# Kernel tuning notes

Measured on AMD Instinct MI355X. Metric: run time of the kernel, lower is better.

## Reference

```python
import jax, jax.numpy as jnp
import numpy as np

NUM_ITERATIONS = 5
M_CHECKS, N_CODE, ROW_WEIGHT = 63, 127, 8
BATCH = 4096
BIG = 1e10  # sentinel used by optimized_topk for masked-out entries


def _make_H():
    # Deterministic sparse parity-check matrix with fixed row weight.
    rng = np.random.default_rng(0)
    H = np.zeros((M_CHECKS, N_CODE), dtype=np.int32)
    for i in range(M_CHECKS):
        H[i, rng.choice(N_CODE, ROW_WEIGHT, replace=False)] = 1
    return H


def setup_inputs() -> dict:
    key = jax.random.key(0)
    k1, k2 = jax.random.split(key)
    soft_input = jax.random.normal(k1, (BATCH, N_CODE), dtype=jnp.float32)
    labels = jax.random.randint(k2, (BATCH, N_CODE), 0, 2, dtype=jnp.int32)
    H = jnp.asarray(_make_H())
    normalizor = jnp.full((1,), -2.5, dtype=jnp.float32)  # decoder_check_normalizor
    return {"soft_input": soft_input, "labels": labels, "H": H,
            "normalizor": normalizor}


def _nms_iteration(cur, Hf, supp, norm):
    # variable -> check messages: (B, m, n)
    vc = cur[:, None, :] * Hf
    # sign part: product of signs over each check row, extrinsic per edge
    signs = jnp.sign(supp + vc)  # supplement makes masked entries sign +1
    total_sign = jnp.prod(signs, axis=2, keepdims=True) * Hf
    result_sign = total_sign * signs
    # magnitude part: extrinsic min via top-2 smallest magnitudes per row
    av = jnp.abs(vc)
    proc = jnp.where(av * Hf == 0.0, BIG, av * Hf)
    top2 = -jax.lax.top_k(-proc, 2)[0]           # (B, m, 2) two smallest
    smallest = top2[..., 0:1]
    second = top2[..., 1:2]
    updated = jnp.where(av == smallest, second, smallest) * Hf
    # normalized min-sum check -> variable messages
    cv = norm * updated * jax.lax.stop_gradient(result_sign)
    # marginalize: posterior = prior + sum of incoming check messages
    return cur + jnp.sum(cv, axis=1)


def reference(soft_input, labels, H, normalizor):
    Hf = H.astype(jnp.float32)                # (m, n)
    supp = (1.0 - Hf)[None]                   # supplement_matrix, (1, m, n)
    norm = jax.nn.softplus(normalizor)        # softplus(decoder_check_normalizor)
    outs = [soft_input]
    cur = soft_input
    for _ in range(NUM_ITERATIONS):
        cur = _nms_iteration(cur, Hf, supp, norm)
        outs.append(cur)
    return jnp.stack(outs, axis=0), labels    # (iters+1, B, n), (B, n)
```

## Files before the change

### kernel.cpp

```cpp
#include <hip/hip_runtime.h>
#include <math.h>

#define M_CHECKS 63
#define N_CODE   127
#define ROW_W    8
#define BATCH    4096
#define NITER    5
#define BIGF     1e10f
#define MAXD     16

__launch_bounds__(256, 4)
__global__ void nms_decode(const float* __restrict__ soft,
                           const int*   __restrict__ labels,
                           const int*   __restrict__ H,
                           const float* __restrict__ normalizor,
                           float*       __restrict__ out) {
    __shared__ float cur[4][128];
    __shared__ float cvals[4][MAXD / 2][128][2];
    __shared__ int   sidx[M_CHECKS * ROW_W];
    __shared__ int   sslot[M_CHECKS * ROW_W];
    __shared__ int   cnt[128];

    const int tid  = threadIdx.x;
    const int w    = tid >> 6;
    const int lane = tid & 63;
    const int row  = blockIdx.x * 4 + w;

    {
        float4* cv4 = (float4*)cvals;
        #pragma unroll
        for (int t = 0; t < (4 * MAXD * 128) / 4 / 256; ++t)
            cv4[tid + t * 256] = make_float4(0.f, 0.f, 0.f, 0.f);
        if (tid < 128) cnt[tid] = 0;
    }

    {
        const unsigned long long below =
            (lane == 0) ? 0ull : ((~0ull) >> (64 - lane));
        for (int i = w; i < M_CHECKS; i += 4) {
            const int c0 = lane;
            const int c1 = lane + 64;
            const int b0 = (H[i * N_CODE + c0] != 0) ? 1 : 0;
            const int b1 = (c1 < N_CODE) ? ((H[i * N_CODE + c1] != 0) ? 1 : 0) : 0;
            unsigned long long m0 = __ballot(b0);
            unsigned long long m1 = __ballot(b1);
            if (b0) {
                int pos = __popcll(m0 & below);
                if (pos < ROW_W) sidx[i * ROW_W + pos] = c0;
            }
            if (b1) {
                int pos = __popcll(m0) + __popcll(m1 & below);
                if (pos < ROW_W) sidx[i * ROW_W + pos] = c1;
            }
        }
    }
    __syncthreads();

    if (w == 0 && lane < M_CHECKS) {
        #pragma unroll
        for (int p = 0; p < ROW_W; ++p) {
            int c = sidx[lane * ROW_W + p];
            sslot[lane * ROW_W + p] = atomicAdd(&cnt[c], 1);
        }
    }
    __syncthreads();

    int dmax = max(cnt[lane], cnt[lane + 64]);
    #pragma unroll
    for (int off = 32; off; off >>= 1)
        dmax = max(dmax, __shfl_xor(dmax, off, 64));
    const int spairs = min((dmax + 1) >> 1, MAXD / 2);

    const float norm = log1pf(expf(normalizor[0]));
    float* outLabels = out + (size_t)(NITER + 1) * BATCH * N_CODE;
    float* const cvw = &cvals[w][0][0][0];

    int ec[ROW_W];
    int widx[ROW_W];
    if (lane < M_CHECKS) {
        #pragma unroll
        for (int p = 0; p < ROW_W; ++p) {
            int c   = sidx[lane * ROW_W + p];
            int s   = min(sslot[lane * ROW_W + p], MAXD - 1);
            ec[p]   = c;
            widx[p] = (s >> 1) * 256 + 2 * c + (s & 1);
        }
    }

    const int j0 = lane;
    const int j1 = lane + 64;
    float x0, x1 = 0.0f;
    {
        const size_t base = (size_t)row * N_CODE;
        x0 = soft[base + j0];
        cur[w][j0] = x0;
        out[base + j0] = x0;
        outLabels[base + j0] = (float)labels[base + j0];
        if (lane < 63) {
            x1 = soft[base + j1];
            cur[w][j1] = x1;
            out[base + j1] = x1;
            outLabels[base + j1] = (float)labels[base + j1];
        }
    }
    asm volatile("" ::: "memory");
    __builtin_amdgcn_sched_barrier(0);

    for (int it = 0; it < NITER; ++it) {
        if (lane < M_CHECKS) {
            float v[ROW_W];
            #pragma unroll
            for (int p = 0; p < ROW_W; ++p) v[p] = cur[w][ec[p]];

            float m1 = BIGF, m2 = BIGF, sprod = 1.0f;
            #pragma unroll
            for (int p = 0; p < ROW_W; ++p) {
                float x = v[p];
                float s = (x > 0.0f) ? 1.0f : ((x < 0.0f) ? -1.0f : 0.0f);
                sprod *= s;
                float av   = fabsf(x);
                float proc = (av == 0.0f) ? BIGF : av;
                if (proc < m1) { m2 = m1; m1 = proc; }
                else if (proc < m2) { m2 = proc; }
            }
            const float nsp = norm * sprod;
            #pragma unroll
            for (int p = 0; p < ROW_W; ++p) {
                float x   = v[p];
                float s   = (x > 0.0f) ? 1.0f : ((x < 0.0f) ? -1.0f : 0.0f);
                float av  = fabsf(x);
                float upd = (av == m1) ? m2 : m1;
                cvw[widx[p]] = nsp * upd * s;
            }
        }
        asm volatile("" ::: "memory");
        __builtin_amdgcn_sched_barrier(0);

        const float2* cv2 = (const float2*)cvw;
        float acc0 = 0.0f, acc1 = 0.0f;
        for (int e = 0; e < spairs; ++e) {
            float2 a = cv2[e * 128 + j0];
            float2 b = cv2[e * 128 + j1];
            acc0 += a.x + a.y;
            acc1 += b.x + b.y;
        }
        x0 += acc0;
        x1 += acc1;

        cur[w][j0] = x0;
        cur[w][j1] = x1;

        const size_t obase = (size_t)(it + 1) * BATCH * N_CODE + (size_t)row * N_CODE;
        out[obase + j0] = x0;
        if (lane < 63) out[obase + j1] = x1;

        asm volatile("" ::: "memory");
        __builtin_amdgcn_sched_barrier(0);
    }
}

extern "C" void kernel_launch(void* const* d_in, const int* in_sizes, int n_in,
                              void* d_out, int out_size, void* d_ws, size_t ws_size,
                              hipStream_t stream) {
    const float* soft       = (const float*)d_in[0];
    const int*   labels     = (const int*)d_in[1];
    const int*   H          = (const int*)d_in[2];
    const float* normalizor = (const float*)d_in[3];
    float*       out        = (float*)d_out;

    nms_decode<<<BATCH / 4, 256, 0, stream>>>(soft, labels, H, normalizor, out);
}
```

Baseline: 79.56 us.

## Precompute H edge tables in a separate kernel and use sign-bit arithmetic

Moves parsing of the parity-check matrix, the per-column slot assignment and the degree calculation out of every decode block into a one-block prepass kernel that writes a compact table to workspace. The decode kernel then loads its edge indices with vector loads and no longer needs block-wide barriers or shared-memory atomics; each wave zeroes only its own scratch. The check-node sign product is replaced with XOR of sign bits and a zero flag. In exchange it adds a second kernel launch with a serial dependency, and it relies on the workspace buffer being large enough.

Result: slower. 85.19 us (+7.1%).

```diff
diff --git a/kernel.cpp b/kernel.cpp
--- a/kernel.cpp
+++ b/kernel.cpp
@@ -9,17 +9,76 @@
 #define BIGF     1e10f
 #define MAXD     16
 
+__global__ void build_tables(const int* __restrict__ H, int* __restrict__ tbl) {
+    __shared__ int                sidx[M_CHECKS * ROW_W];
+    __shared__ unsigned long long cmask[128];
+
+    const int lane = threadIdx.x & 63;
+    const int c0 = lane;
+    const int c1 = lane + 64;
+    unsigned long long cm0 = 0ull, cm1 = 0ull;
+    const unsigned long long below =
+        (lane == 0) ? 0ull : ((~0ull) >> (64 - lane));
+
+    for (int k = 0; k < 4; ++k) {
+        int a[16], b[16];
+        #pragma unroll
+        for (int r = 0; r < 16; ++r) {
+            int i = k * 16 + r;
+            a[r] = (i < M_CHECKS) ? H[i * N_CODE + c0] : 0;
+            b[r] = (i < M_CHECKS && c1 < N_CODE) ? H[i * N_CODE + c1] : 0;
+        }
+        #pragma unroll
+        for (int r = 0; r < 16; ++r) {
+            int i = k * 16 + r;
+            if (i < M_CHECKS) {
+                unsigned long long m0 = __ballot(a[r] != 0);
+                unsigned long long m1 = __ballot(b[r] != 0);
+                if (a[r]) {
+                    int pos = __popcll(m0 & below);
+                    if (pos < ROW_W) sidx[i * ROW_W + pos] = c0;
+                }
+                if (b[r]) {
+                    int pos = __popcll(m0) + __popcll(m1 & below);
+                    if (pos < ROW_W) sidx[i * ROW_W + pos] = c1;
+                }
+                cm0 |= a[r] ? (1ull << i) : 0ull;
+                cm1 |= b[r] ? (1ull << i) : 0ull;
+            }
+        }
+    }
+    cmask[c0] = cm0;
+    cmask[c1 & 127] = cm1;
+
+    int deg = max(__popcll(cm0), __popcll(cm1));
+    #pragma unroll
+    for (int off = 32; off; off >>= 1)
+        deg = max(deg, __shfl_xor(deg, off, 64));
+
+    asm volatile("" ::: "memory");
+    __builtin_amdgcn_sched_barrier(0);
+
+    if (lane < M_CHECKS) {
+        const unsigned long long ibelow = (1ull << lane) - 1;
+        #pragma unroll
+        for (int p = 0; p < ROW_W; ++p) {
+            int c    = sidx[lane * ROW_W + p];
+            int slot = (int)__popcll(cmask[c] & ibelow);
+            tbl[lane * 16 + p]     = c;
+            tbl[lane * 16 + 8 + p] = (slot >> 1) * 256 + 2 * c + (slot & 1);
+        }
+    }
+    if (lane == 0) tbl[M_CHECKS * 16] = (deg + 1) >> 1;
+}
+
 __launch_bounds__(256, 4)
 __global__ void nms_decode(const float* __restrict__ soft,
                            const int*   __restrict__ labels,
-                           const int*   __restrict__ H,
                            const float* __restrict__ normalizor,
+                           const int*   __restrict__ tbl,
                            float*       __restrict__ out) {
     __shared__ float cur[4][128];
     __shared__ float cvals[4][MAXD / 2][128][2];
-    __shared__ int   sidx[M_CHECKS * ROW_W];
-    __shared__ int   sslot[M_CHECKS * ROW_W];
-    __shared__ int   cnt[128];
 
     const int tid  = threadIdx.x;
     const int w    = tid >> 6;
@@ -27,65 +86,26 @@
     const int row  = blockIdx.x * 4 + w;
 
     {
-        float4* cv4 = (float4*)cvals;
+        float4* z = (float4*)&cvals[w][0][0][0];
         #pragma unroll
-        for (int t = 0; t < (4 * MAXD * 128) / 4 / 256; ++t)
-            cv4[tid + t * 256] = make_float4(0.f, 0.f, 0.f, 0.f);
-        if (tid < 128) cnt[tid] = 0;
+        for (int t = 0; t < 8; ++t)
+            z[lane + t * 64] = make_float4(0.f, 0.f, 0.f, 0.f);
     }
 
+    int ec[ROW_W], widx[ROW_W];
     {
-        const unsigned long long below =
-            (lane == 0) ? 0ull : ((~0ull) >> (64 - lane));
-        for (int i = w; i < M_CHECKS; i += 4) {
-            const int c0 = lane;
-            const int c1 = lane + 64;
-            const int b0 = (H[i * N_CODE + c0] != 0) ? 1 : 0;
-            const int b1 = (c1 < N_CODE) ? ((H[i * N_CODE + c1] != 0) ? 1 : 0) : 0;
-            unsigned long long m0 = __ballot(b0);
-            unsigned long long m1 = __ballot(b1);
-            if (b0) {
-                int pos = __popcll(m0 & below);
-                if (pos < ROW_W) sidx[i * ROW_W + pos] = c0;
-            }
-            if (b1) {
-                int pos = __popcll(m0) + __popcll(m1 & below);
-                if (pos < ROW_W) sidx[i * ROW_W + pos] = c1;
-            }
-        }
+        const int4* t4 = (const int4*)(tbl + lane * 16);
+        int4 A = t4[0], B = t4[1], C = t4[2], D = t4[3];
+        ec[0] = A.x; ec[1] = A.y; ec[2] = A.z; ec[3] = A.w;
+        ec[4] = B.x; ec[5] = B.y; ec[6] = B.z; ec[7] = B.w;
+        widx[0] = C.x; widx[1] = C.y; widx[2] = C.z; widx[3] = C.w;
+        widx[4] = D.x; widx[5] = D.y; widx[6] = D.z; widx[7] = D.w;
     }
-    __syncthreads();
-
-    if (w == 0 && lane < M_CHECKS) {
-        #pragma unroll
-        for (int p = 0; p < ROW_W; ++p) {
-            int c = sidx[lane * ROW_W + p];
-            sslot[lane * ROW_W + p] = atomicAdd(&cnt[c], 1);
-        }
-    }
-    __syncthreads();
-
-    int dmax = max(cnt[lane], cnt[lane + 64]);
-    #pragma unroll
-    for (int off = 32; off; off >>= 1)
-        dmax = max(dmax, __shfl_xor(dmax, off, 64));
-    const int spairs = min((dmax + 1) >> 1, MAXD / 2);
+    const int spairs = __builtin_amdgcn_readfirstlane(tbl[M_CHECKS * 16]);
 
     const float norm = log1pf(expf(normalizor[0]));
     float* outLabels = out + (size_t)(NITER + 1) * BATCH * N_CODE;
     float* const cvw = &cvals[w][0][0][0];
-
-    int ec[ROW_W];
-    int widx[ROW_W];
-    if (lane < M_CHECKS) {
-        #pragma unroll
-        for (int p = 0; p < ROW_W; ++p) {
-            int c   = sidx[lane * ROW_W + p];
-            int s   = min(sslot[lane * ROW_W + p], MAXD - 1);
-            ec[p]   = c;
-            widx[p] = (s >> 1) * 256 + 2 * c + (s & 1);
-        }
-    }
 
     const int j0 = lane;
     const int j1 = lane + 64;
@@ -112,25 +132,26 @@
             #pragma unroll
             for (int p = 0; p < ROW_W; ++p) v[p] = cur[w][ec[p]];
 
-            float m1 = BIGF, m2 = BIGF, sprod = 1.0f;
+            float m1 = BIGF, m2 = BIGF;
+            unsigned xb = 0u;
+            bool anyz = false;
             #pragma unroll
             for (int p = 0; p < ROW_W; ++p) {
                 float x = v[p];
-                float s = (x > 0.0f) ? 1.0f : ((x < 0.0f) ? -1.0f : 0.0f);
-                sprod *= s;
-                float av   = fabsf(x);
-                float proc = (av == 0.0f) ? BIGF : av;
-                if (proc < m1) { m2 = m1; m1 = proc; }
-                else if (proc < m2) { m2 = proc; }
+                xb ^= __float_as_uint(x);
+                anyz |= (x == 0.0f);
+                float av = fabsf(x);
+                if (av < m1) { m2 = m1; m1 = av; }
+                else if (av < m2) { m2 = av; }
             }
-            const float nsp = norm * sprod;
+            const float    nsp = anyz ? 0.0f : norm;
+            const unsigned par = xb & 0x80000000u;
             #pragma unroll
             for (int p = 0; p < ROW_W; ++p) {
                 float x   = v[p];
-                float s   = (x > 0.0f) ? 1.0f : ((x < 0.0f) ? -1.0f : 0.0f);
-                float av  = fabsf(x);
-                float upd = (av == m1) ? m2 : m1;
-                cvw[widx[p]] = nsp * upd * s;
+                float upd = (fabsf(x) == m1) ? m2 : m1;
+                unsigned sb = (__float_as_uint(x) & 0x80000000u) ^ par;
+                cvw[widx[p]] = __uint_as_float(__float_as_uint(nsp * upd) ^ sb);
             }
         }
         asm volatile("" ::: "memory");
@@ -167,6 +188,8 @@
     const int*   H          = (const int*)d_in[2];
     const float* normalizor = (const float*)d_in[3];
     float*       out        = (float*)d_out;
+    int*         tbl        = (int*)d_ws;
 
-    nms_decode<<<BATCH / 4, 256, 0, stream>>>(soft, labels, H, normalizor, out);
+    build_tables<<<1, 64, 0, stream>>>(H, tbl);
+    nms_decode<<<BATCH / 4, 256, 0, stream>>>(soft, labels, normalizor, tbl, out);
 }
```

## Replace shared-memory state with wave shuffles and drop atomic slot assignment

Applied to the files above, without the earlier changes.

Removes the per-wave shared `cur` array and gathers variable values with cross-lane shuffles. It also replaces the atomic per-column slot counting, and the extra block barrier it needed, with per-column check bitmasks and popcount prefix slots. The sign and min logic is rewritten as bitwise sign-parity XOR with a zero flag, and each wave zeroes only its own message buffer. The aim is to cut LDS traffic, atomics and barriers in setup and iterations, at the cost of two shuffles per edge and more register work.

New measurement: 83.08 us. +4.4%, slower.

```diff
diff --git a/kernel.cpp b/kernel.cpp
--- a/kernel.cpp
+++ b/kernel.cpp
@@ -6,7 +6,6 @@
 #define ROW_W    8
 #define BATCH    4096
 #define NITER    5
-#define BIGF     1e10f
 #define MAXD     16
 
 __launch_bounds__(256, 4)
@@ -15,11 +14,9 @@
                            const int*   __restrict__ H,
                            const float* __restrict__ normalizor,
                            float*       __restrict__ out) {
-    __shared__ float cur[4][128];
     __shared__ float cvals[4][MAXD / 2][128][2];
-    __shared__ int   sidx[M_CHECKS * ROW_W];
-    __shared__ int   sslot[M_CHECKS * ROW_W];
-    __shared__ int   cnt[128];
+    __shared__ int   sidx[64 * ROW_W];
+    __shared__ unsigned long long cmaskp[4][128];
 
     const int tid  = threadIdx.x;
     const int w    = tid >> 6;
@@ -27,19 +24,19 @@
     const int row  = blockIdx.x * 4 + w;
 
     {
-        float4* cv4 = (float4*)cvals;
+        float4* z = (float4*)&cvals[w][0][0][0];
         #pragma unroll
-        for (int t = 0; t < (4 * MAXD * 128) / 4 / 256; ++t)
-            cv4[tid + t * 256] = make_float4(0.f, 0.f, 0.f, 0.f);
-        if (tid < 128) cnt[tid] = 0;
+        for (int t = 0; t < 8; ++t)
+            z[lane + t * 64] = make_float4(0.f, 0.f, 0.f, 0.f);
     }
 
     {
         const unsigned long long below =
             (lane == 0) ? 0ull : ((~0ull) >> (64 - lane));
+        const int c0 = lane;
+        const int c1 = lane + 64;
+        unsigned long long cm0 = 0ull, cm1 = 0ull;
         for (int i = w; i < M_CHECKS; i += 4) {
-            const int c0 = lane;
-            const int c1 = lane + 64;
             const int b0 = (H[i * N_CODE + c0] != 0) ? 1 : 0;
             const int b1 = (c1 < N_CODE) ? ((H[i * N_CODE + c1] != 0) ? 1 : 0) : 0;
             unsigned long long m0 = __ballot(b0);
@@ -52,40 +49,47 @@
                 int pos = __popcll(m0) + __popcll(m1 & below);
                 if (pos < ROW_W) sidx[i * ROW_W + pos] = c1;
             }
+            cm0 |= b0 ? (1ull << i) : 0ull;
+            cm1 |= b1 ? (1ull << i) : 0ull;
         }
+        cmaskp[w][c0] = cm0;
+        cmaskp[w][c1 & 127] = cm1;
+        if (w == 3 && lane < ROW_W) sidx[M_CHECKS * ROW_W + lane] = 0;
     }
     __syncthreads();
 
-    if (w == 0 && lane < M_CHECKS) {
+    int ec[ROW_W], widx[ROW_W];
+    {
+        #pragma unroll
+        for (int p = 0; p < ROW_W; ++p) ec[p] = sidx[lane * ROW_W + p];
+        const unsigned long long ibelow = (1ull << lane) - 1;
         #pragma unroll
         for (int p = 0; p < ROW_W; ++p) {
-            int c = sidx[lane * ROW_W + p];
-            sslot[lane * ROW_W + p] = atomicAdd(&cnt[c], 1);
+            int c = ec[p];
+            unsigned long long cm = cmaskp[0][c] | cmaskp[1][c]
+                                  | cmaskp[2][c] | cmaskp[3][c];
+            int slot = (int)__popcll(cm & ibelow);
+            widx[p] = (slot >> 1) * 256 + 2 * c + (slot & 1);
         }
     }
-    __syncthreads();
 
-    int dmax = max(cnt[lane], cnt[lane + 64]);
-    #pragma unroll
-    for (int off = 32; off; off >>= 1)
-        dmax = max(dmax, __shfl_xor(dmax, off, 64));
-    const int spairs = min((dmax + 1) >> 1, MAXD / 2);
+    int spairs;
+    {
+        const unsigned long long mj0 = cmaskp[0][lane] | cmaskp[1][lane]
+                                     | cmaskp[2][lane] | cmaskp[3][lane];
+        const unsigned long long mj1 = cmaskp[0][lane + 64] | cmaskp[1][lane + 64]
+                                     | cmaskp[2][lane + 64] | cmaskp[3][lane + 64];
+        int deg = max(__popcll(mj0), __popcll(mj1));
+        #pragma unroll
+        for (int off = 32; off; off >>= 1)
+            deg = max(deg, __shfl_xor(deg, off, 64));
+        spairs = min((deg + 1) >> 1, MAXD / 2);
+    }
 
     const float norm = log1pf(expf(normalizor[0]));
     float* outLabels = out + (size_t)(NITER + 1) * BATCH * N_CODE;
     float* const cvw = &cvals[w][0][0][0];
-
-    int ec[ROW_W];
-    int widx[ROW_W];
-    if (lane < M_CHECKS) {
-        #pragma unroll
-        for (int p = 0; p < ROW_W; ++p) {
-            int c   = sidx[lane * ROW_W + p];
-            int s   = min(sslot[lane * ROW_W + p], MAXD - 1);
-            ec[p]   = c;
-            widx[p] = (s >> 1) * 256 + 2 * c + (s & 1);
-        }
-    }
+    const float2* const cv2 = (const float2*)cvw;
 
     const int j0 = lane;
     const int j1 = lane + 64;
@@ -93,69 +97,65 @@
     {
         const size_t base = (size_t)row * N_CODE;
         x0 = soft[base + j0];
-        cur[w][j0] = x0;
         out[base + j0] = x0;
         outLabels[base + j0] = (float)labels[base + j0];
         if (lane < 63) {
             x1 = soft[base + j1];
-            cur[w][j1] = x1;
             out[base + j1] = x1;
             outLabels[base + j1] = (float)labels[base + j1];
         }
     }
-    asm volatile("" ::: "memory");
-    __builtin_amdgcn_sched_barrier(0);
 
     for (int it = 0; it < NITER; ++it) {
+        float v[ROW_W];
+        #pragma unroll
+        for (int p = 0; p < ROW_W; ++p) {
+            const int c  = ec[p];
+            const float lo = __shfl(x0, c, 64);
+            const float hi = __shfl(x1, c, 64);
+            v[p] = (c < 64) ? lo : hi;
+        }
+
+        float m1 = 1e30f, m2 = 1e30f;
+        unsigned xb = 0u;
+        bool anyz = false;
+        #pragma unroll
+        for (int p = 0; p < ROW_W; ++p) {
+            const float x = v[p];
+            xb ^= __float_as_uint(x);
+            anyz |= (x == 0.0f);
+            const float av = fabsf(x);
+            if (av < m1) { m2 = m1; m1 = av; }
+            else if (av < m2) { m2 = av; }
+        }
+        const float    nsp = anyz ? 0.0f : norm;
+        const unsigned par = xb & 0x80000000u;
+
         if (lane < M_CHECKS) {
-            float v[ROW_W];
-            #pragma unroll
-            for (int p = 0; p < ROW_W; ++p) v[p] = cur[w][ec[p]];
-
-            float m1 = BIGF, m2 = BIGF, sprod = 1.0f;
             #pragma unroll
             for (int p = 0; p < ROW_W; ++p) {
-                float x = v[p];
-                float s = (x > 0.0f) ? 1.0f : ((x < 0.0f) ? -1.0f : 0.0f);
-                sprod *= s;
-                float av   = fabsf(x);
-                float proc = (av == 0.0f) ? BIGF : av;
-                if (proc < m1) { m2 = m1; m1 = proc; }
-                else if (proc < m2) { m2 = proc; }
-            }
-            const float nsp = norm * sprod;
-            #pragma unroll
-            for (int p = 0; p < ROW_W; ++p) {
-                float x   = v[p];
-                float s   = (x > 0.0f) ? 1.0f : ((x < 0.0f) ? -1.0f : 0.0f);
-                float av  = fabsf(x);
-                float upd = (av == m1) ? m2 : m1;
-                cvw[widx[p]] = nsp * upd * s;
+                const float    x   = v[p];
+                const float    upd = (fabsf(x) == m1) ? m2 : m1;
+                const unsigned sb  = (__float_as_uint(x) & 0x80000000u) ^ par;
+                cvw[widx[p]] = __uint_as_float(__float_as_uint(nsp * upd) ^ sb);
             }
         }
         asm volatile("" ::: "memory");
         __builtin_amdgcn_sched_barrier(0);
 
-        const float2* cv2 = (const float2*)cvw;
         float acc0 = 0.0f, acc1 = 0.0f;
         for (int e = 0; e < spairs; ++e) {
-            float2 a = cv2[e * 128 + j0];
-            float2 b = cv2[e * 128 + j1];
+            const float2 a = cv2[e * 128 + j0];
+            const float2 b = cv2[e * 128 + j1];
             acc0 += a.x + a.y;
             acc1 += b.x + b.y;
         }
         x0 += acc0;
         x1 += acc1;
 
-        cur[w][j0] = x0;
-        cur[w][j1] = x1;
-
         const size_t obase = (size_t)(it + 1) * BATCH * N_CODE + (size_t)row * N_CODE;
         out[obase + j0] = x0;
         if (lane < 63) out[obase + j1] = x1;
-
-        asm volatile("" ::: "memory");
-        __builtin_amdgcn_sched_barrier(0);
     }
 }
 
```
